# Kernel optimization log

Measured on AMD Instinct MI355X. Metric: run time of the kernel, lower is better.

## Reference

```python
import jax, jax.numpy as jnp
import numpy as np

BETA = 0.9
THRESHOLD = 1.0
ATAN_ALPHA = 2.0  # snntorch ATan surrogate default


def setup_inputs() -> dict:
    key = jax.random.key(0)
    k1, k2 = jax.random.split(key)
    T, B, NI, NO = 100, 128, 2048, 1024
    x = jax.random.normal(k1, (T, B, NI), dtype=jnp.float32)
    # Kaiming-uniform-ish init like nn.Linear
    bound = 1.0 / np.sqrt(NI)
    W = jax.random.uniform(k2, (NO, NI), dtype=jnp.float32, minval=-bound, maxval=bound)
    return {"x": x, "W": W}


def _heaviside(u):
    return (u > 0).astype(u.dtype)


def reference(x, W):
    # cur[t] = x[t] @ W.T for all timesteps at once: [T, B, NO]
    cur = jnp.einsum('tbi,oi->tbo', x, W)

    def step(mem, cur_t):
        # snntorch Leaky (reset_mechanism='subtract'):
        #   reset = heaviside(mem_prev - threshold)   (detached)
        #   mem   = beta * mem_prev + cur - reset * threshold
        #   spk   = heaviside(mem - threshold)
        reset = _heaviside(mem - THRESHOLD)
        mem_new = BETA * mem + cur_t - reset * THRESHOLD
        spk = _heaviside(mem_new - THRESHOLD)
        return mem_new, (spk, mem_new)

    mem0 = jnp.zeros(cur.shape[1:], dtype=cur.dtype)  # [B, NO]
    _, (spk_rec, mem_rec) = jax.lax.scan(step, mem0, cur)
    return spk_rec, mem_rec
```

## Files before the change

kernel.cpp:

```cpp
#include <hip/hip_runtime.h>

#define T_STEPS 100
#define BATCH   128
#define NI      2048
#define NO      1024
#define M_TOT   (T_STEPS * BATCH)
#define TOTAL   (T_STEPS * BATCH * NO)
#define BNTOT   (BATCH * NO)
#define X_ELEMS (M_TOT * NI)

#define BMf 64
#define BNf 128
#define BKf 32
#define LDA (BMf + 4)
#define LDB (BNf + 4)
#define NXB (NO / BNf)
#define NYB (M_TOT/BMf)
#define YPX (NYB / 8)

__global__ __launch_bounds__(256) void gemm_512fold(const float* __restrict__ X,
                                                    const float* __restrict__ W,
                                                    float* __restrict__ curOut) {
    __shared__ float As[BKf][LDA];
    __shared__ float Bs[BKf][LDB];

    const int orig = blockIdx.x;
    const int k_x  = orig & 7;
    const int q    = orig >> 3;
    const int m0   = (k_x * YPX + (q >> 3)) * BMf;
    const int n0   = (q & 7) * BNf;

    const int tid = threadIdx.x;
    const int tx  = tid & 15;
    const int ty  = tid >> 4;

    const int ar = tid >> 2;
    const int ak = (tid & 3) * 4;
    const int br = tid >> 1;
    const int bk = (tid & 1) * 4;

    float ch[4][8]  = {};
    float tot[4][8] = {};

    #pragma unroll 1
    for (int k0 = 0; k0 < NI; k0 += BKf) {
        if (k0 == 512 || k0 == 1024 || k0 == 1536) {
            #pragma unroll
            for (int i = 0; i < 4; ++i)
                #pragma unroll
                for (int j = 0; j < 8; ++j) {
                    tot[i][j] = __fadd_rn(tot[i][j], ch[i][j]);
                    ch[i][j]  = 0.0f;
                }
        }

        {
            const float4 fa0 = *reinterpret_cast<const float4*>(
                &X[(size_t)(m0 + ar) * NI + k0 + ak]);
            const float4 fa1 = *reinterpret_cast<const float4*>(
                &X[(size_t)(m0 + ar) * NI + k0 + ak + 16]);
            As[ak + 0][ar] = fa0.x;  As[ak + 1][ar] = fa0.y;
            As[ak + 2][ar] = fa0.z;  As[ak + 3][ar] = fa0.w;
            As[ak + 16][ar] = fa1.x; As[ak + 17][ar] = fa1.y;
            As[ak + 18][ar] = fa1.z; As[ak + 19][ar] = fa1.w;
            #pragma unroll
            for (int qq = 0; qq < 4; ++qq) {
                const int kb = bk + qq * 8;
                const float4 fb = *reinterpret_cast<const float4*>(
                    &W[(size_t)(n0 + br) * NI + k0 + kb]);
                Bs[kb + 0][br] = fb.x; Bs[kb + 1][br] = fb.y;
                Bs[kb + 2][br] = fb.z; Bs[kb + 3][br] = fb.w;
            }
        }
        __syncthreads();

        #pragma unroll
        for (int kk = 0; kk < BKf; ++kk) {
            float a[4], b[8];
            *reinterpret_cast<float4*>(&a[0]) =
                *reinterpret_cast<const float4*>(&As[kk][ty * 4]);
            *reinterpret_cast<float4*>(&b[0]) =
                *reinterpret_cast<const float4*>(&Bs[kk][tx * 4]);
            *reinterpret_cast<float4*>(&b[4]) =
                *reinterpret_cast<const float4*>(&Bs[kk][64 + tx * 4]);
            #pragma unroll
            for (int i = 0; i < 4; ++i)
                #pragma unroll
                for (int j = 0; j < 8; ++j)
                    ch[i][j] = __fmaf_rn(a[i], b[j], ch[i][j]);
        }
        __syncthreads();
    }

    #pragma unroll
    for (int i = 0; i < 4; ++i) {
        const size_t rowbase = (size_t)(m0 + ty * 4 + i) * NO + n0;
        #pragma unroll
        for (int h = 0; h < 2; ++h) {
            float4 v;
            v.x = __fadd_rn(tot[i][h * 4 + 0], ch[i][h * 4 + 0]);
            v.y = __fadd_rn(tot[i][h * 4 + 1], ch[i][h * 4 + 1]);
            v.z = __fadd_rn(tot[i][h * 4 + 2], ch[i][h * 4 + 2]);
            v.w = __fadd_rn(tot[i][h * 4 + 3], ch[i][h * 4 + 3]);
            *reinterpret_cast<float4*>(&curOut[rowbase + h * 64 + tx * 4]) = v;
        }
    }
}

__global__ __launch_bounds__(256) void lif_scan(float* __restrict__ spk,
                                                float* __restrict__ memf) {
    const int idx = (blockIdx.x * blockDim.x + threadIdx.x) * 4;
    float4 mem = make_float4(0.f, 0.f, 0.f, 0.f);
    for (int t = 0; t < T_STEPS; ++t) {
        const size_t i = (size_t)t * BNTOT + idx;
        const float4 cur = *reinterpret_cast<const float4*>(&memf[i]);
        float4 spkv;
        #define STEP(c)                                                   \
        {                                                                 \
            const float reset = (mem.c > 1.0f) ? 1.0f : 0.0f;             \
            float tmp = __fmul_rn(0.9f, mem.c);                           \
            tmp = __fadd_rn(tmp, cur.c);                                  \
            mem.c = __fsub_rn(tmp, reset);                                \
            spkv.c = (mem.c > 1.0f) ? 1.0f : 0.0f;                        \
        }
        STEP(x) STEP(y) STEP(z) STEP(w)
        #undef STEP
        *reinterpret_cast<float4*>(&spk[i])  = spkv;
        *reinterpret_cast<float4*>(&memf[i]) = mem;
    }
}

extern "C" void kernel_launch(void* const* d_in, const int* in_sizes, int n_in,
                              void* d_out, int out_size, void* d_ws, size_t ws_size,
                              hipStream_t stream) {
    const float* X;
    const float* W;
    if (in_sizes[0] == X_ELEMS) { X = (const float*)d_in[0]; W = (const float*)d_in[1]; }
    else                        { X = (const float*)d_in[1]; W = (const float*)d_in[0]; }

    float* spk  = (float*)d_out;
    float* memf = spk + TOTAL;

    gemm_512fold<<<NXB * NYB, 256, 0, stream>>>(X, W, memf);

    lif_scan<<<BNTOT / 4 / 256, 256, 0, stream>>>(spk, memf);
}
```

Before: 715.9 us.

## Split GEMM K dimension into four chains and fold partials in scan

The GEMM is split along K into four independent 512-wide chunks, each launched as its own set of blocks (four times the grid), writing partial sums into the two output buffers and two workspace buffers. The LIF scan kernel then sums the four partials in the same fixed order before running the recurrence. This raises parallelism and occupancy for the GEMM, since each block's K loop is a quarter as long. The cost is writing and reading three extra full-size partial tensors, about 157 MB more traffic per partial pass. It only runs when the workspace is large enough; otherwise it falls back to the old path.

```diff
diff --git a/kernel.cpp b/kernel.cpp
--- a/kernel.cpp
+++ b/kernel.cpp
@@ -18,17 +18,25 @@
 #define NYB (M_TOT/BMf)
 #define YPX (NYB / 8)
 
-__global__ __launch_bounds__(256) void gemm_512fold(const float* __restrict__ X,
-                                                    const float* __restrict__ W,
-                                                    float* __restrict__ curOut) {
+__global__ __launch_bounds__(256) void gemm_chain512(const float* __restrict__ X,
+                                                     const float* __restrict__ W,
+                                                     float* __restrict__ p0,
+                                                     float* __restrict__ p1,
+                                                     float* __restrict__ p2,
+                                                     float* __restrict__ p3) {
     __shared__ float As[BKf][LDA];
     __shared__ float Bs[BKf][LDB];
 
-    const int orig = blockIdx.x;
-    const int k_x  = orig & 7;
-    const int q    = orig >> 3;
-    const int m0   = (k_x * YPX + (q >> 3)) * BMf;
-    const int n0   = (q & 7) * BNf;
+    const int orig  = blockIdx.x;
+    const int xcd   = orig & 7;
+    const int q     = orig >> 3;
+    const int n0    = (q & 7) * BNf;
+    const int t     = q >> 3;
+    const int chain = t / 25;
+    const int my    = t - chain * 25;
+    const int m0    = (xcd * YPX + my) * BMf;
+    const int kbase = chain * 512;
+    float* out = (chain == 0) ? p0 : (chain == 1) ? p1 : (chain == 2) ? p2 : p3;
 
     const int tid = threadIdx.x;
     const int tx  = tid & 15;
@@ -39,21 +47,10 @@
     const int br = tid >> 1;
     const int bk = (tid & 1) * 4;
 
-    float ch[4][8]  = {};
-    float tot[4][8] = {};
+    float ch[4][8] = {};
 
     #pragma unroll 1
-    for (int k0 = 0; k0 < NI; k0 += BKf) {
-        if (k0 == 512 || k0 == 1024 || k0 == 1536) {
-            #pragma unroll
-            for (int i = 0; i < 4; ++i)
-                #pragma unroll
-                for (int j = 0; j < 8; ++j) {
-                    tot[i][j] = __fadd_rn(tot[i][j], ch[i][j]);
-                    ch[i][j]  = 0.0f;
-                }
-        }
-
+    for (int k0 = kbase; k0 < kbase + 512; k0 += BKf) {
         {
             const float4 fa0 = *reinterpret_cast<const float4*>(
                 &X[(size_t)(m0 + ar) * NI + k0 + ak]);
@@ -92,6 +89,115 @@
         __syncthreads();
     }
 
+    #pragma unroll
+    for (int i = 0; i < 4; ++i) {
+        const size_t rowbase = (size_t)(m0 + ty * 4 + i) * NO + n0;
+        #pragma unroll
+        for (int h = 0; h < 2; ++h) {
+            float4 v;
+            v.x = ch[i][h * 4 + 0]; v.y = ch[i][h * 4 + 1];
+            v.z = ch[i][h * 4 + 2]; v.w = ch[i][h * 4 + 3];
+            *reinterpret_cast<float4*>(&out[rowbase + h * 64 + tx * 4]) = v;
+        }
+    }
+}
+
+__global__ __launch_bounds__(256) void fold_scan(float* __restrict__ spk,
+                                                 float* __restrict__ memf,
+                                                 const float* __restrict__ p2,
+                                                 const float* __restrict__ p3) {
+    const int idx = (blockIdx.x * blockDim.x + threadIdx.x) * 4;
+    float4 mem = make_float4(0.f, 0.f, 0.f, 0.f);
+    for (int t = 0; t < T_STEPS; ++t) {
+        const size_t i = (size_t)t * BNTOT + idx;
+        const float4 c0 = *reinterpret_cast<const float4*>(&spk[i]);
+        const float4 c1 = *reinterpret_cast<const float4*>(&memf[i]);
+        const float4 c2 = *reinterpret_cast<const float4*>(&p2[i]);
+        const float4 c3 = *reinterpret_cast<const float4*>(&p3[i]);
+        float4 spkv;
+        #define STEP(c)                                                     \
+        {                                                                   \
+            const float cur = __fadd_rn(__fadd_rn(__fadd_rn(c0.c, c1.c),    \
+                                                  c2.c), c3.c);             \
+            const float reset = (mem.c > 1.0f) ? 1.0f : 0.0f;               \
+            float tmp = __fmul_rn(0.9f, mem.c);                             \
+            tmp = __fadd_rn(tmp, cur);                                      \
+            mem.c = __fsub_rn(tmp, reset);                                  \
+            spkv.c = (mem.c > 1.0f) ? 1.0f : 0.0f;                          \
+        }
+        STEP(x) STEP(y) STEP(z) STEP(w)
+        #undef STEP
+        *reinterpret_cast<float4*>(&spk[i])  = spkv;
+        *reinterpret_cast<float4*>(&memf[i]) = mem;
+    }
+}
+
+__global__ __launch_bounds__(256) void gemm_512fold(const float* __restrict__ X,
+                                                    const float* __restrict__ W,
+                                                    float* __restrict__ curOut) {
+    __shared__ float As[BKf][LDA];
+    __shared__ float Bs[BKf][LDB];
+    const int orig = blockIdx.x;
+    const int k_x  = orig & 7;
+    const int q    = orig >> 3;
+    const int m0   = (k_x * YPX + (q >> 3)) * BMf;
+    const int n0   = (q & 7) * BNf;
+    const int tid = threadIdx.x;
+    const int tx  = tid & 15;
+    const int ty  = tid >> 4;
+    const int ar = tid >> 2;
+    const int ak = (tid & 3) * 4;
+    const int br = tid >> 1;
+    const int bk = (tid & 1) * 4;
+    float ch[4][8]  = {};
+    float tot[4][8] = {};
+    #pragma unroll 1
+    for (int k0 = 0; k0 < NI; k0 += BKf) {
+        if (k0 == 512 || k0 == 1024 || k0 == 1536) {
+            #pragma unroll
+            for (int i = 0; i < 4; ++i)
+                #pragma unroll
+                for (int j = 0; j < 8; ++j) {
+                    tot[i][j] = __fadd_rn(tot[i][j], ch[i][j]);
+                    ch[i][j]  = 0.0f;
+                }
+        }
+        {
+            const float4 fa0 = *reinterpret_cast<const float4*>(
+                &X[(size_t)(m0 + ar) * NI + k0 + ak]);
+            const float4 fa1 = *reinterpret_cast<const float4*>(
+                &X[(size_t)(m0 + ar) * NI + k0 + ak + 16]);
+            As[ak + 0][ar] = fa0.x;  As[ak + 1][ar] = fa0.y;
+            As[ak + 2][ar] = fa0.z;  As[ak + 3][ar] = fa0.w;
+            As[ak + 16][ar] = fa1.x; As[ak + 17][ar] = fa1.y;
+            As[ak + 18][ar] = fa1.z; As[ak + 19][ar] = fa1.w;
+            #pragma unroll
+            for (int qq = 0; qq < 4; ++qq) {
+                const int kb = bk + qq * 8;
+                const float4 fb = *reinterpret_cast<const float4*>(
+                    &W[(size_t)(n0 + br) * NI + k0 + kb]);
+                Bs[kb + 0][br] = fb.x; Bs[kb + 1][br] = fb.y;
+                Bs[kb + 2][br] = fb.z; Bs[kb + 3][br] = fb.w;
+            }
+        }
+        __syncthreads();
+        #pragma unroll
+        for (int kk = 0; kk < BKf; ++kk) {
+            float a[4], b[8];
+            *reinterpret_cast<float4*>(&a[0]) =
+                *reinterpret_cast<const float4*>(&As[kk][ty * 4]);
+            *reinterpret_cast<float4*>(&b[0]) =
+                *reinterpret_cast<const float4*>(&Bs[kk][tx * 4]);
+            *reinterpret_cast<float4*>(&b[4]) =
+                *reinterpret_cast<const float4*>(&Bs[kk][64 + tx * 4]);
+            #pragma unroll
+            for (int i = 0; i < 4; ++i)
+                #pragma unroll
+                for (int j = 0; j < 8; ++j)
+                    ch[i][j] = __fmaf_rn(a[i], b[j], ch[i][j]);
+        }
+        __syncthreads();
+    }
     #pragma unroll
     for (int i = 0; i < 4; ++i) {
         const size_t rowbase = (size_t)(m0 + ty * 4 + i) * NO + n0;
@@ -141,7 +247,13 @@
     float* spk  = (float*)d_out;
     float* memf = spk + TOTAL;
 
-    gemm_512fold<<<NXB * NYB, 256, 0, stream>>>(X, W, memf);
-
-    lif_scan<<<BNTOT / 4 / 256, 256, 0, stream>>>(spk, memf);
-}
+    if (ws_size >= (size_t)2 * TOTAL * sizeof(float)) {
+        float* p2 = (float*)d_ws;
+        float* p3 = p2 + TOTAL;
+        gemm_chain512<<<4 * NXB * NYB, 256, 0, stream>>>(X, W, spk, memf, p2, p3);
+        fold_scan<<<BNTOT / 4 / 256, 256, 0, stream>>>(spk, memf, p2, p3);
+    } else {
+        gemm_512fold<<<NXB * NYB, 256, 0, stream>>>(X, W, memf);
+        lif_scan<<<BNTOT / 4 / 256, 256, 0, stream>>>(spk, memf);
+    }
+}
```

New measurement: 653.5 us. 8.7% less time.
